# Kernel optimization log

Hardware: AMD Instinct MI355X
Metric: run time of the kernel (lower is better)

The kernel has to match this reference:

```python
import jax, jax.numpy as jnp
import numpy as np

D_MODEL = 1024
NUM_HEADS = 16
D_K = D_MODEL // NUM_HEADS
B, T_Q, T_K = 4, 2048, 2048


def setup_inputs() -> dict:
    key = jax.random.key(0)
    ks = jax.random.split(key, 12)
    s = 1.0 / np.sqrt(D_MODEL)
    inp = {
        "query": jax.random.normal(ks[0], (B, T_Q, D_MODEL), jnp.float32),
        "key": jax.random.normal(ks[1], (B, T_K, D_MODEL), jnp.float32),
        "value": jax.random.normal(ks[2], (B, T_K, D_MODEL), jnp.float32),
        # no padded keys (all zeros = all attendable)
        "key_padding_mask": jnp.zeros((B, T_K), jnp.int32),
        # causal mask from the docstring: nonzero = disallowed (strict upper triangle)
        "attention_mask": jnp.triu(jnp.ones((T_Q, T_K), jnp.int32), k=1)[None],
        # nn.Linear params: y = x @ W.T + b
        "W_q": jax.random.uniform(ks[3], (D_MODEL, D_MODEL), jnp.float32, -s, s),
        "b_q": jax.random.uniform(ks[4], (D_MODEL,), jnp.float32, -s, s),
        "W_k": jax.random.uniform(ks[5], (D_MODEL, D_MODEL), jnp.float32, -s, s),
        "b_k": jax.random.uniform(ks[6], (D_MODEL,), jnp.float32, -s, s),
        "W_v": jax.random.uniform(ks[7], (D_MODEL, D_MODEL), jnp.float32, -s, s),
        "b_v": jax.random.uniform(ks[8], (D_MODEL,), jnp.float32, -s, s),
        "W_o": jax.random.uniform(ks[9], (D_MODEL, D_MODEL), jnp.float32, -s, s),
        "b_o": jax.random.uniform(ks[10], (D_MODEL,), jnp.float32, -s, s),
    }
    return inp


def reference(query, key, value, key_padding_mask, attention_mask,
              W_q, b_q, W_k, b_k, W_v, b_v, W_o, b_o):
    b, tq, _ = query.shape
    tk = key.shape[1]
    # QKV projections (nn.Linear: x @ W.T + b), split heads -> B, H, T, d_k
    def proj(x, W, bias, t):
        y = jnp.einsum('btd,ed->bte', x, W) + bias
        return y.reshape(b, t, NUM_HEADS, D_K).transpose(0, 2, 1, 3)
    q = proj(query, W_q, b_q, tq)
    k = proj(key, W_k, b_k, tk)
    v = proj(value, W_v, b_v, tk)

    min_val = jnp.finfo(q.dtype).min
    # scores: B, H, T_q, T_k
    S = jnp.einsum('bhqd,bhkd->bhqk', q, k) / jnp.sqrt(jnp.array(D_K, q.dtype))
    S = jnp.where(key_padding_mask[:, None, None, :] != 0, min_val, S)
    S = jnp.where(attention_mask[:, None, :, :] == 1, min_val, S)
    att = jax.nn.softmax(S, axis=3)
    x = jnp.einsum('bhqk,bhkd->bhqd', att, v)
    x = x.transpose(0, 2, 1, 3).reshape(b, tq, D_MODEL)
    return jnp.einsum('btd,ed->bte', x, W_o) + b_o
```

## Files before the change

### kernel.cpp

```cpp
#include <hip/hip_runtime.h>
#include <hip/hip_bf16.h>
#include <stdint.h>

typedef uint16_t u16;
typedef __attribute__((ext_vector_type(8))) __bf16 bf16x8;
typedef __attribute__((ext_vector_type(4))) float f32x4;
typedef __attribute__((ext_vector_type(4))) u16 u16x4;

#define MFMA16(a, b, c) __builtin_amdgcn_mfma_f32_16x16x32_bf16(a, b, c, 0, 0, 0)
#define GL16(gp, lp)                                                            \
  __builtin_amdgcn_global_load_lds(                                             \
      (const __attribute__((address_space(1))) void*)(gp),                      \
      (__attribute__((address_space(3))) void*)(lp), 16, 0, 0)

__device__ __forceinline__ u16 f2bf(float f) {
  uint32_t u = __builtin_bit_cast(uint32_t, f);
  u += 0x7FFFu + ((u >> 16) & 1u);
  return (u16)(u >> 16);
}

__global__ __launch_bounds__(256) void cast_f32_bf16(const float* __restrict__ in,
                                                     u16* __restrict__ out, int n8) {
  int i = blockIdx.x * blockDim.x + threadIdx.x;
  if (i >= n8) return;
  const float4* p = (const float4*)in + 2 * (size_t)i;
  float4 a = p[0], b = p[1];
  u16x4 lo = {f2bf(a.x), f2bf(a.y), f2bf(a.z), f2bf(a.w)};
  u16x4 hi = {f2bf(b.x), f2bf(b.y), f2bf(b.z), f2bf(b.w)};
  u16x4* o = (u16x4*)(out + 8 * (size_t)i);
  o[0] = lo;
  o[1] = hi;
}

template <int V>
__global__ __launch_bounds__(256) void gemm_bt(const u16* __restrict__ A,
                                               const u16* __restrict__ W,
                                               const float* __restrict__ bias,
                                               void* __restrict__ outp) {
  constexpr int K = 1024;
  __shared__ u16 lsA[128 * 32];
  __shared__ u16 lsB[128 * 32];
  const int t = threadIdx.x;
  const int lane = t & 63, wid = t >> 6;
  const int l15 = lane & 15, lhi = lane >> 4;
  const int wr = wid >> 1, wc = wid & 1;
  const int m0 = blockIdx.x * 128, n0 = blockIdx.y * 128;
  const int arow = t >> 2, acol = (t & 3) * 8;
  const u16* gA = A + (size_t)(m0 + arow) * K + acol;
  const u16* gB = W + (size_t)(n0 + arow) * K + acol;
  u16* lA0 = lsA + wid * 512;
  u16* lB0 = lsB + wid * 512;

  f32x4 acc[4][4] = {};
  for (int k0 = 0; k0 < K; k0 += 32) {
    GL16(gA + k0, lA0);
    GL16(gA + 64 * K + k0, lA0 + 2048);
    GL16(gB + k0, lB0);
    GL16(gB + 64 * K + k0, lB0 + 2048);
    __syncthreads();
    bf16x8 af[4], bfr[4];
#pragma unroll
    for (int mb = 0; mb < 4; ++mb)
      af[mb] = *(const bf16x8*)&lsA[(wr * 64 + mb * 16 + l15) * 32 + lhi * 8];
#pragma unroll
    for (int nb = 0; nb < 4; ++nb)
      bfr[nb] = *(const bf16x8*)&lsB[(wc * 64 + nb * 16 + l15) * 32 + lhi * 8];
#pragma unroll
    for (int mb = 0; mb < 4; ++mb)
#pragma unroll
      for (int nb = 0; nb < 4; ++nb)
        acc[mb][nb] = MFMA16(af[mb], bfr[nb], acc[mb][nb]);
    __syncthreads();
  }

  const int mbase = m0 + wr * 64, nbase = n0 + wc * 64;
#pragma unroll
  for (int nb = 0; nb < 4; ++nb) {
    const int n = nbase + nb * 16 + l15;
    const float bv = bias[n];
#pragma unroll
    for (int mb = 0; mb < 4; ++mb) {
      const int mrow = mbase + mb * 16 + lhi * 4;
      if constexpr (V == 0) {
        u16* out = (u16*)outp;
#pragma unroll
        for (int r = 0; r < 4; ++r) {
          int m = mrow + r;
          int b = m >> 11, tt = m & 2047, h = n >> 6, d = n & 63;
          out[((size_t)((b * 16 + h) * 2048 + tt)) * 64 + d] = f2bf(acc[mb][nb][r] + bv);
        }
      } else if constexpr (V == 1) {
        u16* out = (u16*)outp;
        u16x4 pk;
#pragma unroll
        for (int r = 0; r < 4; ++r) pk[r] = f2bf(acc[mb][nb][r] + bv);
        int b = mrow >> 11, tt = mrow & 2047, h = n >> 6, d = n & 63;
        *(u16x4*)&out[((size_t)((b * 16 + h) * 64 + d)) * 2048 + tt] = pk;
      } else {
        float* out = (float*)outp;
#pragma unroll
        for (int r = 0; r < 4; ++r) {
          int m = mrow + r;
          out[(size_t)m * 1024 + n] = acc[mb][nb][r] + bv;
        }
      }
    }
  }
}

__global__ __launch_bounds__(256) void flash_attn(const u16* __restrict__ Qh,
                                                  const u16* __restrict__ Kh,
                                                  const u16* __restrict__ Vt,
                                                  u16* __restrict__ X) {
  const int bh = blockIdx.y;
  const int q0 = blockIdx.x * 128;
  const int t = threadIdx.x, lane = t & 63, wid = t >> 6;
  const int l15 = lane & 15, lhi = lane >> 4;
  __shared__ u16 ldsP[4 * 32 * 64];
  u16* myP = ldsP + wid * 2048;
  const int qw = q0 + wid * 32;
  const u16* Qb = Qh + (size_t)bh * 2048 * 64;
  const u16* Kb = Kh + (size_t)bh * 2048 * 64;
  const u16* Vb = Vt + (size_t)bh * 64 * 2048;

  bf16x8 qf[2][2];
#pragma unroll
  for (int rg = 0; rg < 2; ++rg)
#pragma unroll
    for (int ks = 0; ks < 2; ++ks)
      qf[rg][ks] = *(const bf16x8*)&Qb[(size_t)(qw + rg * 16 + l15) * 64 + ks * 32 + lhi * 8];

  f32x4 o[2][4] = {};
  float mrun[2][4], lrun[2][4];
#pragma unroll
  for (int rg = 0; rg < 2; ++rg)
#pragma unroll
    for (int r = 0; r < 4; ++r) {
      mrun[rg][r] = -1e38f;
      lrun[rg][r] = 0.f;
    }
  const f32x4 z4 = {0.f, 0.f, 0.f, 0.f};

  const int ktend = qw + 32;
  for (int kt0 = 0; kt0 < ktend; kt0 += 64) {
    bf16x8 kf[4][2];
#pragma unroll
    for (int nb = 0; nb < 4; ++nb)
#pragma unroll
      for (int ks = 0; ks < 2; ++ks)
        kf[nb][ks] = *(const bf16x8*)&Kb[(size_t)(kt0 + nb * 16 + l15) * 64 + ks * 32 + lhi * 8];

#pragma unroll
    for (int rg = 0; rg < 2; ++rg) {
      f32x4 s[4];
#pragma unroll
      for (int nb = 0; nb < 4; ++nb) {
        s[nb] = MFMA16(qf[rg][0], kf[nb][0], z4);
        s[nb] = MFMA16(qf[rg][1], kf[nb][1], s[nb]);
      }
      const int row0 = rg * 16 + lhi * 4;
      const int qrow0 = qw + row0;
#pragma unroll
      for (int r = 0; r < 4; ++r) {
        const int q = qrow0 + r;
#pragma unroll
        for (int nb = 0; nb < 4; ++nb) {
          float v = s[nb][r] * 0.125f;
          int kt = kt0 + nb * 16 + l15;
          s[nb][r] = (kt > q) ? -3.0e38f : v;
        }
        float rm = fmaxf(fmaxf(s[0][r], s[1][r]), fmaxf(s[2][r], s[3][r]));
#pragma unroll
        for (int off = 1; off < 16; off <<= 1) rm = fmaxf(rm, __shfl_xor(rm, off));
        const float mo = mrun[rg][r];
        const float mn = fmaxf(mo, rm);
        const float corr = __expf(mo - mn);
        mrun[rg][r] = mn;
        float ps = 0.f;
        const int row = row0 + r;
#pragma unroll
        for (int nb = 0; nb < 4; ++nb) {
          float p = __expf(s[nb][r] - mn);
          ps += p;
          int idx = (row * 64 + nb * 16 + l15) ^ ((row & 7) << 3);
          myP[idx] = f2bf(p);
        }
#pragma unroll
        for (int off = 1; off < 16; off <<= 1) ps += __shfl_xor(ps, off);
        lrun[rg][r] = lrun[rg][r] * corr + ps;
#pragma unroll
        for (int db = 0; db < 4; ++db) o[rg][db][r] *= corr;
      }
    }

    bf16x8 vf[4][2];
#pragma unroll
    for (int db = 0; db < 4; ++db)
#pragma unroll
      for (int ks = 0; ks < 2; ++ks)
        vf[db][ks] = *(const bf16x8*)&Vb[(size_t)(db * 16 + l15) * 2048 + kt0 + ks * 32 + lhi * 8];
#pragma unroll
    for (int rg = 0; rg < 2; ++rg)
#pragma unroll
      for (int ks = 0; ks < 2; ++ks) {
        const int row = rg * 16 + l15;
        const int idx = (row * 64 + ks * 32 + lhi * 8) ^ ((row & 7) << 3);
        bf16x8 pa = *(const bf16x8*)&myP[idx];
#pragma unroll
        for (int db = 0; db < 4; ++db) o[rg][db] = MFMA16(pa, vf[db][ks], o[rg][db]);
      }
  }

  const int b = bh >> 4, h = bh & 15;
#pragma unroll
  for (int rg = 0; rg < 2; ++rg)
#pragma unroll
    for (int r = 0; r < 4; ++r) {
      const float inv = 1.f / lrun[rg][r];
      const int q = qw + rg * 16 + lhi * 4 + r;
#pragma unroll
      for (int db = 0; db < 4; ++db) {
        const int d = db * 16 + l15;
        X[(size_t)(b * 2048 + q) * 1024 + h * 64 + d] = f2bf(o[rg][db][r] * inv);
      }
    }
}

extern "C" void kernel_launch(void* const* d_in, const int* in_sizes, int n_in,
                              void* d_out, int out_size, void* d_ws, size_t ws_size,
                              hipStream_t stream) {
  const float* q_in = (const float*)d_in[0];
  const float* k_in = (const float*)d_in[1];
  const float* v_in = (const float*)d_in[2];
  const float* Wq = (const float*)d_in[5];
  const float* bq = (const float*)d_in[6];
  const float* Wk = (const float*)d_in[7];
  const float* bk = (const float*)d_in[8];
  const float* Wv = (const float*)d_in[9];
  const float* bv = (const float*)d_in[10];
  const float* Wo = (const float*)d_in[11];
  const float* bo = (const float*)d_in[12];

  uint8_t* ws = (uint8_t*)d_ws;
  u16* qbf = (u16*)(ws);
  u16* kbf = (u16*)(ws + (16ull << 20));
  u16* vbf = (u16*)(ws + (32ull << 20));
  u16* Qhb = (u16*)(ws + (48ull << 20));
  u16* wqb = (u16*)(ws + (64ull << 20));
  u16* wkb = (u16*)(ws + (66ull << 20));
  u16* wvb = (u16*)(ws + (68ull << 20));
  u16* wob = (u16*)(ws + (70ull << 20));
  u16* Khb = (u16*)d_out;
  u16* Vtb = (u16*)d_out + (8ull << 20);
  u16* Xbf = qbf;

  const int nQKV = 4 * 2048 * 1024;
  const int nW = 1024 * 1024;
  hipLaunchKernelGGL(cast_f32_bf16, dim3(nQKV / 8 / 256), dim3(256), 0, stream, q_in, qbf, nQKV / 8);
  hipLaunchKernelGGL(cast_f32_bf16, dim3(nQKV / 8 / 256), dim3(256), 0, stream, k_in, kbf, nQKV / 8);
  hipLaunchKernelGGL(cast_f32_bf16, dim3(nQKV / 8 / 256), dim3(256), 0, stream, v_in, vbf, nQKV / 8);
  hipLaunchKernelGGL(cast_f32_bf16, dim3(nW / 8 / 256), dim3(256), 0, stream, Wq, wqb, nW / 8);
  hipLaunchKernelGGL(cast_f32_bf16, dim3(nW / 8 / 256), dim3(256), 0, stream, Wk, wkb, nW / 8);
  hipLaunchKernelGGL(cast_f32_bf16, dim3(nW / 8 / 256), dim3(256), 0, stream, Wv, wvb, nW / 8);
  hipLaunchKernelGGL(cast_f32_bf16, dim3(nW / 8 / 256), dim3(256), 0, stream, Wo, wob, nW / 8);

  dim3 gg(64, 8), gb(256);
  hipLaunchKernelGGL((gemm_bt<0>), gg, gb, 0, stream, qbf, wqb, bq, (void*)Qhb);
  hipLaunchKernelGGL((gemm_bt<0>), gg, gb, 0, stream, kbf, wkb, bk, (void*)Khb);
  hipLaunchKernelGGL((gemm_bt<1>), gg, gb, 0, stream, vbf, wvb, bv, (void*)Vtb);
  hipLaunchKernelGGL(flash_attn, dim3(16, 64), dim3(256), 0, stream, Qhb, Khb, Vtb, Xbf);
  hipLaunchKernelGGL((gemm_bt<2>), gg, gb, 0, stream, Xbf, wob, bo, d_out);
}
```

Before: 529.5 us.

## Split flash attention into single-wave blocks scheduled heaviest-first; batch cast launches

Flash attention now runs one 64-thread wavefront per block, each handling 32 query rows, with blocks ordered in reverse so the longest causal rows start first. This is meant to improve load balance across CUs under the causal mask, which leaves some waves with far more key blocks than others. The seven cast launches are merged into two multi-segment launches to cut launch overhead. In exchange, each block is smaller, so scheduling overhead per block rises, and any sharing between waves in the same block is lost.

```diff
diff --git a/kernel.cpp b/kernel.cpp
--- a/kernel.cpp
+++ b/kernel.cpp
@@ -19,8 +19,15 @@
   return (u16)(u >> 16);
 }
 
-__global__ __launch_bounds__(256) void cast_f32_bf16(const float* __restrict__ in,
-                                                     u16* __restrict__ out, int n8) {
+struct CastJobs {
+  const float* s[4];
+  u16* d[4];
+};
+
+__global__ __launch_bounds__(256) void cast_multi(CastJobs c, int n8) {
+  const int seg = blockIdx.y;
+  const float* __restrict__ in = c.s[seg];
+  u16* __restrict__ out = c.d[seg];
   int i = blockIdx.x * blockDim.x + threadIdx.x;
   if (i >= n8) return;
   const float4* p = (const float4*)in + 2 * (size_t)i;
@@ -108,17 +115,15 @@
   }
 }
 
-__global__ __launch_bounds__(256) void flash_attn(const u16* __restrict__ Qh,
-                                                  const u16* __restrict__ Kh,
-                                                  const u16* __restrict__ Vt,
-                                                  u16* __restrict__ X) {
+__global__ __launch_bounds__(64) void flash_attn(const u16* __restrict__ Qh,
+                                                 const u16* __restrict__ Kh,
+                                                 const u16* __restrict__ Vt,
+                                                 u16* __restrict__ X) {
   const int bh = blockIdx.y;
-  const int q0 = blockIdx.x * 128;
-  const int t = threadIdx.x, lane = t & 63, wid = t >> 6;
+  const int lane = threadIdx.x & 63;
   const int l15 = lane & 15, lhi = lane >> 4;
-  __shared__ u16 ldsP[4 * 32 * 64];
-  u16* myP = ldsP + wid * 2048;
-  const int qw = q0 + wid * 32;
+  __shared__ u16 myP[32 * 64];
+  const int qw = (63 - (int)blockIdx.x) * 32;
   const u16* Qb = Qh + (size_t)bh * 2048 * 64;
   const u16* Kb = Kh + (size_t)bh * 2048 * 64;
   const u16* Vb = Vt + (size_t)bh * 64 * 2048;
@@ -254,20 +259,23 @@
   u16* Vtb = (u16*)d_out + (8ull << 20);
   u16* Xbf = qbf;
 
-  const int nQKV = 4 * 2048 * 1024;
-  const int nW = 1024 * 1024;
-  hipLaunchKernelGGL(cast_f32_bf16, dim3(nQKV / 8 / 256), dim3(256), 0, stream, q_in, qbf, nQKV / 8);
-  hipLaunchKernelGGL(cast_f32_bf16, dim3(nQKV / 8 / 256), dim3(256), 0, stream, k_in, kbf, nQKV / 8);
-  hipLaunchKernelGGL(cast_f32_bf16, dim3(nQKV / 8 / 256), dim3(256), 0, stream, v_in, vbf, nQKV / 8);
-  hipLaunchKernelGGL(cast_f32_bf16, dim3(nW / 8 / 256), dim3(256), 0, stream, Wq, wqb, nW / 8);
-  hipLaunchKernelGGL(cast_f32_bf16, dim3(nW / 8 / 256), dim3(256), 0, stream, Wk, wkb, nW / 8);
-  hipLaunchKernelGGL(cast_f32_bf16, dim3(nW / 8 / 256), dim3(256), 0, stream, Wv, wvb, nW / 8);
-  hipLaunchKernelGGL(cast_f32_bf16, dim3(nW / 8 / 256), dim3(256), 0, stream, Wo, wob, nW / 8);
+  const int nQKV8 = 4 * 2048 * 1024 / 8;
+  const int nW8 = 1024 * 1024 / 8;
+
+  CastJobs cq;
+  cq.s[0] = q_in; cq.s[1] = k_in; cq.s[2] = v_in; cq.s[3] = q_in;
+  cq.d[0] = qbf;  cq.d[1] = kbf;  cq.d[2] = vbf;  cq.d[3] = qbf;
+  hipLaunchKernelGGL(cast_multi, dim3(nQKV8 / 256, 3), dim3(256), 0, stream, cq, nQKV8);
+
+  CastJobs cw;
+  cw.s[0] = Wq;  cw.s[1] = Wk;  cw.s[2] = Wv;  cw.s[3] = Wo;
+  cw.d[0] = wqb; cw.d[1] = wkb; cw.d[2] = wvb; cw.d[3] = wob;
+  hipLaunchKernelGGL(cast_multi, dim3(nW8 / 256, 4), dim3(256), 0, stream, cw, nW8);
 
   dim3 gg(64, 8), gb(256);
   hipLaunchKernelGGL((gemm_bt<0>), gg, gb, 0, stream, qbf, wqb, bq, (void*)Qhb);
   hipLaunchKernelGGL((gemm_bt<0>), gg, gb, 0, stream, kbf, wkb, bk, (void*)Khb);
   hipLaunchKernelGGL((gemm_bt<1>), gg, gb, 0, stream, vbf, wvb, bv, (void*)Vtb);
-  hipLaunchKernelGGL(flash_attn, dim3(16, 64), dim3(256), 0, stream, Qhb, Khb, Vtb, Xbf);
+  hipLaunchKernelGGL(flash_attn, dim3(64, 64), dim3(64), 0, stream, Qhb, Khb, Vtb, Xbf);
   hipLaunchKernelGGL((gemm_bt<2>), gg, gb, 0, stream, Xbf, wob, bo, d_out);
 }
```

After: 504.2 us. 1.05x faster.
